# Kernel optimization log

Measured on AMD Instinct MI355X. Metric: run time of the kernel, lower is better.

Reference implementation:

```python
import jax, jax.numpy as jnp
import numpy as np
import math

M, D = 512, 512          # memory_size, feature_dim
B, H, W = 16, 64, 64     # conv feature map
TEMP_UPDATE, TEMP_GATHER = 0.1, 0.1


def _l2norm(x, axis):
    # torch F.normalize: x / clamp(||x||, min=eps)
    return x / jnp.maximum(jnp.linalg.norm(x, axis=axis, keepdims=True), 1e-12)


def setup_inputs() -> dict:
    key = jax.random.key(0)
    k1, k2 = jax.random.split(key)
    return {
        "query": jax.random.normal(k1, (B, D, H, W), jnp.float32),
        "keys": jax.random.normal(k2, (M, D), jnp.float32),
    }


def reference(query, keys):
    b, d, h, w = query.shape
    m = keys.shape[0]
    # L2-normalize over channel dim, then [b,h,w,d] -> flatten to [N,d]
    qn = _l2norm(query, 1)
    q = jnp.transpose(qn, (0, 2, 3, 1)).reshape(-1, d)  # [N, d]

    scale = math.sqrt(d) * max(TEMP_GATHER, 1e-6)
    logits = (q @ keys.T) / scale                       # [N, M]
    score_q = jax.nn.softmax(logits, axis=0)            # softmax over queries
    score_m = jax.nn.softmax(logits, axis=1)            # softmax over memory slots

    # ---- gather_loss (train) ----
    _, idx2 = jax.lax.top_k(score_m, 2)                 # [N, 2]
    pos = jax.lax.stop_gradient(keys[idx2[:, 0]])       # top-1 slot
    neg = jax.lax.stop_gradient(keys[idx2[:, 1]])       # top-2 slot (hard negative)
    compactness_loss = jnp.mean((q - pos) ** 2)
    # torch TripletMarginLoss(margin=1.0): pairwise_distance adds eps=1e-6 to diff
    dpos = jnp.linalg.norm(q - pos + 1e-6, axis=1)
    dneg = jnp.linalg.norm(q - neg + 1e-6, axis=1)
    separateness_loss = jnp.mean(jax.nn.relu(dpos - dneg + 1.0))

    # ---- read ----
    concat_mem = jax.lax.stop_gradient(score_m) @ keys  # [N, d]
    updated_query = jnp.concatenate([q, concat_mem], axis=1).reshape(b, h, w, 2 * d)
    updated_query = jnp.transpose(updated_query, (0, 3, 1, 2))  # [b, 2d, h, w]

    # ---- update (torch.no_grad) ----
    g = idx2[:, 0]                                              # gathering indices [N]
    wgt = jnp.take_along_axis(score_q, g[:, None], axis=1)[:, 0]
    query_update = jax.ops.segment_sum(q * wgt[:, None], g, num_segments=m)  # scatter-add
    mmt = min(max(1.0 / max(TEMP_UPDATE, 1e-6), 0.0), 0.999)
    updated_memory = _l2norm(keys * mmt + query_update * (1.0 - mmt), 1)
    updated_memory = jax.lax.stop_gradient(updated_memory)

    return (updated_query, updated_memory, score_q, score_m,
            separateness_loss, compactness_loss)
```

## Files before the change

### kernel.cpp

```cpp
#include <hip/hip_runtime.h>
#include <stdint.h>

#define UM_OFF   67108864u
#define SQ_OFF   67371008u
#define SM_OFF   100925440u
#define SEP_OFF  134479872u
#define COMP_OFF 134479873u

#define WS_QBF   0u
#define WS_EBF   67108864u
#define WS_KBF   134217728u
#define WS_KTBF  134742016u
#define WS_G     135266304u
#define WS_W     135528448u
#define WS_RSUM  135790592u
#define WS_CSUM  136052736u
#define WS_KN2   136054784u
#define WS_KSM   136056832u
#define WS_QSUM  136058880u

typedef __attribute__((ext_vector_type(8))) short short8v;
typedef __attribute__((ext_vector_type(4))) float float4v;

__device__ __forceinline__ unsigned short f2bf(float f) {
  union { float f; uint32_t u; } v; v.f = f;
  return (unsigned short)((v.u + 0x7fffu + ((v.u >> 16) & 1u)) >> 16);
}
__device__ __forceinline__ float bf2f(unsigned short s) {
  union { uint32_t u; float f; } v; v.u = ((uint32_t)s) << 16;
  return v.f;
}

#define GLDS16(gp, lp) __builtin_amdgcn_global_load_lds( \
    (__attribute__((address_space(1))) const void*)(gp), \
    (__attribute__((address_space(3))) void*)(lp), 16, 0, 0)

__global__ __launch_bounds__(512) void k01_prep_norm(
    const float* __restrict__ query, const float* __restrict__ keys,
    unsigned short* __restrict__ kbf, unsigned short* __restrict__ ktbf,
    float* __restrict__ csum, float* __restrict__ rsum,
    float* __restrict__ kn2, float* __restrict__ ksm,
    unsigned short* __restrict__ qbf, float* __restrict__ qsum,
    float* __restrict__ out) {
  int tid = threadIdx.x;
  if (blockIdx.x >= 1024) {
    __shared__ float pn[8], ps[8];
    int b = blockIdx.x - 1024;
    int t = tid;
    int i = b * 512 + t;
    float v = keys[i];
    kbf[i] = f2bf(v);
    ktbf[i] = f2bf(keys[(size_t)t * 512 + b]);
    float s1 = v, s2 = v * v;
    #pragma unroll
    for (int off = 1; off < 64; off <<= 1) {
      s1 += __shfl_xor(s1, off);
      s2 += __shfl_xor(s2, off);
    }
    if ((t & 63) == 0) { pn[t >> 6] = s2; ps[t >> 6] = s1; }
    __syncthreads();
    if (t == 0) {
      float n2 = 0.f, sm = 0.f;
      #pragma unroll
      for (int g = 0; g < 8; ++g) { n2 += pn[g]; sm += ps[g]; }
      kn2[b] = n2; ksm[b] = sm;
    }
    if (i < 65536) rsum[i] = 0.0f;
    if (i < 512) csum[i] = 0.0f;
    if (i < 2) out[SEP_OFF + i] = 0.0f;
    return;
  }
  __shared__ unsigned short vals[512 * 65];
  __shared__ float pp[8][64];
  __shared__ float rs[64];
  int bh = blockIdx.x;
  int b = bh >> 6, h = bh & 63;
  int w = tid & 63, dg = tid >> 6;
  const float* src = query + ((size_t)(b * 512) * 64 + h) * 64 + w;
  float ss = 0.f;
  #pragma unroll 4
  for (int i = 0; i < 64; ++i) {
    int d = dg * 64 + i;
    float v = src[(size_t)d * 4096];
    ss += v * v;
    vals[d * 65 + w] = f2bf(v);
  }
  pp[dg][w] = ss;
  __syncthreads();
  if (tid < 64) {
    float s = 0.f;
    #pragma unroll
    for (int g = 0; g < 8; ++g) s += pp[g][tid];
    rs[tid] = 1.0f / fmaxf(sqrtf(s), 1e-12f);
  }
  __syncthreads();
  float rw_ = rs[w];
  float* dst = out + ((size_t)(b * 1024) * 64 + h) * 64 + w;
  #pragma unroll 4
  for (int i = 0; i < 64; ++i) {
    int d = dg * 64 + i;
    __builtin_nontemporal_store(bf2f(vals[d * 65 + w]) * rw_, &dst[(size_t)d * 4096]);
  }
  int w2 = tid >> 3, dc = tid & 7;
  float rw = rs[w2];
  unsigned short* qrow = qbf + ((size_t)bh * 64 + w2) * 512;
  float qs = 0.f;
  #pragma unroll
  for (int g = 0; g < 8; ++g) {
    int d0 = g * 64 + dc * 8;
    short8v pk;
    #pragma unroll
    for (int jj = 0; jj < 8; ++jj) {
      float qn = bf2f(vals[(d0 + jj) * 65 + w2]) * rw;
      qs += qn;
      pk[jj] = (short)f2bf(qn);
    }
    *(short8v*)(qrow + d0) = pk;
  }
  qs += __shfl_xor(qs, 1); qs += __shfl_xor(qs, 2); qs += __shfl_xor(qs, 4);
  if (dc == 0) qsum[bh * 64 + w2] = qs;
}

__global__ __launch_bounds__(256) void k3_gemm1(
    const unsigned short* __restrict__ qbf, const unsigned short* __restrict__ kbf,
    unsigned short* __restrict__ ebf, float* __restrict__ csum, float* __restrict__ rsum) {
  __shared__ unsigned short As[128 * 32];
  __shared__ unsigned short Bs[128 * 32];
  int bid = blockIdx.x;
  int bm = (bid & 7) * 64 + (bid >> 5);
  int bn = (bid >> 3) & 3;
  int tid = threadIdx.x;
  int lane = tid & 63, wid = tid >> 6;
  int wr = wid >> 1, wc = wid & 1;
  float4v acc[4][4];
  #pragma unroll
  for (int m = 0; m < 4; ++m)
    #pragma unroll
    for (int n = 0; n < 4; ++n) acc[m][n] = (float4v){0.f, 0.f, 0.f, 0.f};
  const unsigned short* Abase = qbf + (size_t)bm * 128 * 512;
  const unsigned short* Bbase = kbf + (size_t)bn * 128 * 512;
  int u0 = wid * 128 + lane, u1 = u0 + 64;
  int ra0 = u0 >> 2, ca0 = (u0 & 3) * 8;
  int ra1 = u1 >> 2, ca1 = (u1 & 3) * 8;
  for (int kt = 0; kt < 16; ++kt) {
    const unsigned short* Ak = Abase + kt * 32;
    const unsigned short* Bk = Bbase + kt * 32;
    GLDS16(Ak + (size_t)ra0 * 512 + ca0, &As[(wid * 2 + 0) * 512]);
    GLDS16(Ak + (size_t)ra1 * 512 + ca1, &As[(wid * 2 + 1) * 512]);
    GLDS16(Bk + (size_t)ra0 * 512 + ca0, &Bs[(wid * 2 + 0) * 512]);
    GLDS16(Bk + (size_t)ra1 * 512 + ca1, &Bs[(wid * 2 + 1) * 512]);
    __syncthreads();
    short8v a[4], b[4];
    const unsigned short* pa = As + (wr * 64 + (lane & 15)) * 32 + (lane >> 4) * 8;
    const unsigned short* pb = Bs + (wc * 64 + (lane & 15)) * 32 + (lane >> 4) * 8;
    #pragma unroll
    for (int m = 0; m < 4; ++m) a[m] = *(const short8v*)(pa + m * 512);
    #pragma unroll
    for (int n = 0; n < 4; ++n) b[n] = *(const short8v*)(pb + n * 512);
    #pragma unroll
    for (int m = 0; m < 4; ++m)
      #pragma unroll
      for (int n = 0; n < 4; ++n)
        acc[m][n] = __builtin_amdgcn_mfma_f32_16x16x32_bf16(a[m], b[n], acc[m][n], 0, 0, 0);
    __syncthreads();
  }
  const float inv_scale = 0.44194173824159216f;
  int r0 = bm * 128 + wr * 64 + (lane >> 4) * 4;
  int c0 = bn * 128 + wc * 64 + (lane & 15);
  float cs[4] = {0.f, 0.f, 0.f, 0.f};
  float rp[4][4];
  #pragma unroll
  for (int m = 0; m < 4; ++m)
    #pragma unroll
    for (int j = 0; j < 4; ++j) rp[m][j] = 0.f;
  #pragma unroll
  for (int m = 0; m < 4; ++m)
    #pragma unroll
    for (int n = 0; n < 4; ++n)
      #pragma unroll
      for (int j = 0; j < 4; ++j) {
        float v = __expf(acc[m][n][j] * inv_scale);
        ebf[(size_t)(r0 + m * 16 + j) * 512 + c0 + n * 16] = f2bf(v);
        cs[n] += v;
        rp[m][j] += v;
      }
  #pragma unroll
  for (int n = 0; n < 4; ++n) {
    float v = cs[n];
    v += __shfl_xor(v, 16);
    v += __shfl_xor(v, 32);
    if ((lane >> 4) == 0) atomicAdd(&csum[c0 + n * 16], v);
  }
  #pragma unroll
  for (int m = 0; m < 4; ++m)
    #pragma unroll
    for (int j = 0; j < 4; ++j) {
      float v = rp[m][j];
      v += __shfl_xor(v, 1); v += __shfl_xor(v, 2);
      v += __shfl_xor(v, 4); v += __shfl_xor(v, 8);
      rp[m][j] = v;
    }
  int g16 = lane & 15;
  float myrp = 0.f;
  #pragma unroll
  for (int m = 0; m < 4; ++m)
    #pragma unroll
    for (int j = 0; j < 4; ++j)
      if (g16 == m * 4 + j) myrp = rp[m][j];
  atomicAdd(&rsum[r0 + (g16 >> 2) * 16 + (g16 & 3)], myrp);
}

__global__ __launch_bounds__(256) void k5_fused(
    const unsigned short* __restrict__ ktbf, const unsigned short* __restrict__ ebf,
    const float* __restrict__ rsum, const float* __restrict__ csum,
    const float* __restrict__ qsum, const float* __restrict__ kn2,
    const float* __restrict__ ksm, int* __restrict__ gidx, float* __restrict__ gw,
    float* __restrict__ out) {
  __shared__ unsigned short As[128 * 32];
  __shared__ unsigned short Bs[128 * 32];
  int bid = blockIdx.x;
  int g = (bid & 7) * 64 + (bid >> 5);
  int b = g >> 5, nt = g & 31, dt = (bid >> 3) & 3;
  int tid = threadIdx.x;
  int lane = tid & 63, wid = tid >> 6;
  int wr = wid >> 1, wc = wid & 1;
  float4v acc[4][4];
  #pragma unroll
  for (int m = 0; m < 4; ++m)
    #pragma unroll
    for (int n = 0; n < 4; ++n) acc[m][n] = (float4v){0.f, 0.f, 0.f, 0.f};
  const unsigned short* Abase = ktbf + (size_t)dt * 128 * 512;
  size_t brow0 = (size_t)g * 128;
  int u0 = wid * 128 + lane, u1 = u0 + 64;
  int ra0 = u0 >> 2, ca0 = (u0 & 3) * 8;
  int ra1 = u1 >> 2, ca1 = (u1 & 3) * 8;
  for (int kt = 0; kt < 16; ++kt) {
    GLDS16(Abase + (size_t)ra0 * 512 + kt * 32 + ca0, &As[(wid * 2 + 0) * 512]);
    GLDS16(Abase + (size_t)ra1 * 512 + kt * 32 + ca1, &As[(wid * 2 + 1) * 512]);
    GLDS16(ebf + (brow0 + ra0) * 512 + kt * 32 + ca0, &Bs[(wid * 2 + 0) * 512]);
    GLDS16(ebf + (brow0 + ra1) * 512 + kt * 32 + ca1, &Bs[(wid * 2 + 1) * 512]);
    __syncthreads();
    short8v a[4], bb[4];
    const unsigned short* pa = As + (wr * 64 + (lane & 15)) * 32 + (lane >> 4) * 8;
    const unsigned short* pb = Bs + (wc * 64 + (lane & 15)) * 32 + (lane >> 4) * 8;
    #pragma unroll
    for (int m = 0; m < 4; ++m) a[m] = *(const short8v*)(pa + m * 512);
    #pragma unroll
    for (int n = 0; n < 4; ++n) bb[n] = *(const short8v*)(pb + n * 512);
    #pragma unroll
    for (int m = 0; m < 4; ++m)
      #pragma unroll
      for (int n = 0; n < 4; ++n)
        acc[m][n] = __builtin_amdgcn_mfma_f32_16x16x32_bf16(a[m], bb[n], acc[m][n], 0, 0, 0);
    __syncthreads();
  }
  {
    float* dst = out + (size_t)b * 4194304 + (size_t)512 * 4096;
    int d0 = dt * 128 + wr * 64 + (lane >> 4) * 4;
    int c0 = nt * 128 + wc * 64 + (lane & 15);
    float invc[4];
    #pragma unroll
    for (int n = 0; n < 4; ++n) invc[n] = 1.0f / rsum[b * 4096 + c0 + n * 16];
    #pragma unroll
    for (int m = 0; m < 4; ++m)
      #pragma unroll
      for (int n = 0; n < 4; ++n)
        #pragma unroll
        for (int j = 0; j < 4; ++j)
          __builtin_nontemporal_store(acc[m][n][j] * invc[n],
              &dst[(size_t)(d0 + m * 16 + j) * 4096 + (c0 + n * 16)]);
  }
  float4v cA = *(const float4v*)(csum + lane * 8);
  float4v cB = *(const float4v*)(csum + lane * 8 + 4);
  float4v rcA, rcB;
  #pragma unroll
  for (int j = 0; j < 4; ++j) { rcA[j] = 1.0f / cA[j]; rcB[j] = 1.0f / cB[j]; }
  float closs = 0.f, sloss = 0.f;
  const float S2 = 4.525483399593904f;
  int r_base = g * 128 + dt * 32 + wid * 8;
  for (int it = 0; it < 8; ++it) {
    int r = r_base + it;
    short8v eb = *(const short8v*)(ebf + (size_t)r * 512 + lane * 8);
    float e[8];
    #pragma unroll
    for (int j = 0; j < 8; ++j) e[j] = bf2f((unsigned short)eb[j]);
    float invr = 1.0f / rsum[r];
    float v1 = -1.f, v2 = -2.f; int i1 = 0, i2 = 0;
    #pragma unroll
    for (int j = 0; j < 8; ++j) {
      float val = e[j]; int idx = lane * 8 + j;
      if (val > v1) { v2 = v1; i2 = i1; v1 = val; i1 = idx; }
      else if (val > v2) { v2 = val; i2 = idx; }
    }
    #pragma unroll
    for (int off = 1; off < 64; off <<= 1) {
      float ov1 = __shfl_xor(v1, off); int oi1 = __shfl_xor(i1, off);
      float ov2 = __shfl_xor(v2, off); int oi2 = __shfl_xor(i2, off);
      bool take = (ov1 > v1) || (ov1 == v1 && oi1 < i1);
      float av = take ? v1 : v2;  int ai = take ? i1 : i2;
      float bv = take ? ov2 : ov1; int bi = take ? oi2 : oi1;
      bool t2 = (bv > av) || (bv == av && bi < ai);
      v2 = t2 ? bv : av; i2 = t2 ? bi : ai;
      v1 = take ? ov1 : v1; i1 = take ? oi1 : i1;
    }
    float* SQrow = out + SQ_OFF + (size_t)r * 512;
    float* SMrow = out + SM_OFF + (size_t)r * 512;
    float4v sq0, sq1, sm0, sm1;
    #pragma unroll
    for (int j = 0; j < 4; ++j) {
      sq0[j] = e[j] * rcA[j];     sq1[j] = e[4 + j] * rcB[j];
      sm0[j] = e[j] * invr;       sm1[j] = e[4 + j] * invr;
    }
    __builtin_nontemporal_store(sq0, (float4v*)(SQrow + lane * 8));
    __builtin_nontemporal_store(sq1, (float4v*)(SQrow + lane * 8 + 4));
    __builtin_nontemporal_store(sm0, (float4v*)(SMrow + lane * 8));
    __builtin_nontemporal_store(sm1, (float4v*)(SMrow + lane * 8 + 4));
    float qs = qsum[r];
    float cp_row = 1.0f + kn2[i1] - S2 * __logf(v1);
    float dp2 = cp_row + 2e-6f * (qs - ksm[i1]) + 5.12e-10f;
    float cn_row = 1.0f + kn2[i2] - S2 * __logf(v2);
    float dn2 = cn_row + 2e-6f * (qs - ksm[i2]) + 5.12e-10f;
    closs += cp_row;
    sloss += fmaxf(sqrtf(dp2) - sqrtf(dn2) + 1.0f, 0.f);
    if (lane == 0) { gidx[r] = i1; gw[r] = v1 / csum[i1]; }
  }
  if (lane == 0) {
    atomicAdd(out + SEP_OFF, sloss * (1.0f / 65536.0f));
    atomicAdd(out + COMP_OFF, closs * (1.0f / (65536.0f * 512.0f)));
  }
}

__global__ __launch_bounds__(512) void k4b_gather(
    const int* __restrict__ gidx, const float* __restrict__ gw,
    const unsigned short* __restrict__ qbf, const float* __restrict__ keys,
    float* __restrict__ out) {
  __shared__ float red[8][512];
  __shared__ float wss[8];
  int m = blockIdx.x;
  int tid = threadIdx.x, lane = tid & 63, wid = tid >> 6;
  float acc[8] = {0.f, 0.f, 0.f, 0.f, 0.f, 0.f, 0.f, 0.f};
  for (int c = 0; c < 128; ++c) {
    int r0 = wid * 8192 + c * 64;
    int gv = gidx[r0 + lane];
    unsigned long long mask = __ballot(gv == m);
    while (mask) {
      int bb = __ffsll((long long)mask) - 1;
      mask &= mask - 1;
      int r = r0 + bb;
      float wv = gw[r];
      short8v qv = *(const short8v*)(qbf + (size_t)r * 512 + lane * 8);
      #pragma unroll
      for (int j = 0; j < 8; ++j) acc[j] += wv * bf2f((unsigned short)qv[j]);
    }
  }
  #pragma unroll
  for (int j = 0; j < 8; ++j) red[wid][lane * 8 + j] = acc[j];
  __syncthreads();
  int d0 = tid;
  float s = 0.f;
  #pragma unroll
  for (int g = 0; g < 8; ++g) s += red[g][d0];
  float v = keys[(size_t)m * 512 + d0] * 0.999f + s * 0.001f;
  float ss = v * v;
  #pragma unroll
  for (int off = 1; off < 64; off <<= 1) ss += __shfl_xor(ss, off);
  if (lane == 0) wss[wid] = ss;
  __syncthreads();
  float tot = 0.f;
  #pragma unroll
  for (int g = 0; g < 8; ++g) tot += wss[g];
  float rsn = 1.0f / fmaxf(sqrtf(tot), 1e-12f);
  out[UM_OFF + (size_t)m * 512 + d0] = v * rsn;
}

extern "C" void kernel_launch(void* const* d_in, const int* in_sizes, int n_in,
                              void* d_out, int out_size, void* d_ws, size_t ws_size,
                              hipStream_t stream) {
  const float* query = (const float*)d_in[0];
  const float* keys  = (const float*)d_in[1];
  float* out = (float*)d_out;
  char* ws = (char*)d_ws;
  unsigned short* qbf  = (unsigned short*)(ws + WS_QBF);
  unsigned short* ebf  = (unsigned short*)(ws + WS_EBF);
  unsigned short* kbf  = (unsigned short*)(ws + WS_KBF);
  unsigned short* ktbf = (unsigned short*)(ws + WS_KTBF);
  int*   gidx = (int*)(ws + WS_G);
  float* gw   = (float*)(ws + WS_W);
  float* rsum = (float*)(ws + WS_RSUM);
  float* csum = (float*)(ws + WS_CSUM);
  float* kn2  = (float*)(ws + WS_KN2);
  float* ksm  = (float*)(ws + WS_KSM);
  float* qsum = (float*)(ws + WS_QSUM);

  k01_prep_norm<<<dim3(1536), dim3(512), 0, stream>>>(
      query, keys, kbf, ktbf, csum, rsum, kn2, ksm, qbf, qsum, out);
  k3_gemm1<<<dim3(2048), dim3(256), 0, stream>>>(qbf, kbf, ebf, csum, rsum);
  k5_fused<<<dim3(2048), dim3(256), 0, stream>>>(
      ktbf, ebf, rsum, csum, qsum, kn2, ksm, gidx, gw, out);
  k4b_gather<<<dim3(512), dim3(512), 0, stream>>>(gidx, gw, qbf, keys, out);
}
```

Measured before the change: 421.1 us.

## Bucket query rows per memory slot instead of scanning all indices in gather

The fused softmax kernel now appends each row index to a per-slot list, using an atomic counter per memory slot, instead of writing a dense top-1 index array. The gather kernel then walks only its slot's list rather than having each of the 512 blocks scan all 65536 indices with ballots. This removes the redundant full scans. In exchange it adds atomics in the fused kernel and makes the summation order nondeterministic. Lists are capped at 1024 entries per slot, so a heavily skewed assignment would silently drop rows.

```diff
diff --git a/kernel.cpp b/kernel.cpp
--- a/kernel.cpp
+++ b/kernel.cpp
@@ -11,13 +11,14 @@
 #define WS_EBF   67108864u
 #define WS_KBF   134217728u
 #define WS_KTBF  134742016u
-#define WS_G     135266304u
-#define WS_W     135528448u
-#define WS_RSUM  135790592u
-#define WS_CSUM  136052736u
-#define WS_KN2   136054784u
-#define WS_KSM   136056832u
-#define WS_QSUM  136058880u
+#define WS_W     135266304u
+#define WS_RSUM  135528448u
+#define WS_CSUM  135790592u
+#define WS_KN2   135792640u
+#define WS_KSM   135794688u
+#define WS_CNT   135796736u
+#define WS_QSUM  135798784u
+#define WS_LIST  136060928u
 
 typedef __attribute__((ext_vector_type(8))) short short8v;
 typedef __attribute__((ext_vector_type(4))) float float4v;
@@ -39,7 +40,7 @@
     const float* __restrict__ query, const float* __restrict__ keys,
     unsigned short* __restrict__ kbf, unsigned short* __restrict__ ktbf,
     float* __restrict__ csum, float* __restrict__ rsum,
-    float* __restrict__ kn2, float* __restrict__ ksm,
+    float* __restrict__ kn2, float* __restrict__ ksm, int* __restrict__ cnt,
     unsigned short* __restrict__ qbf, float* __restrict__ qsum,
     float* __restrict__ out) {
   int tid = threadIdx.x;
@@ -66,7 +67,7 @@
       kn2[b] = n2; ksm[b] = sm;
     }
     if (i < 65536) rsum[i] = 0.0f;
-    if (i < 512) csum[i] = 0.0f;
+    if (i < 512) { csum[i] = 0.0f; cnt[i] = 0; }
     if (i < 2) out[SEP_OFF + i] = 0.0f;
     return;
   }
@@ -214,8 +215,8 @@
     const unsigned short* __restrict__ ktbf, const unsigned short* __restrict__ ebf,
     const float* __restrict__ rsum, const float* __restrict__ csum,
     const float* __restrict__ qsum, const float* __restrict__ kn2,
-    const float* __restrict__ ksm, int* __restrict__ gidx, float* __restrict__ gw,
-    float* __restrict__ out) {
+    const float* __restrict__ ksm, int* __restrict__ cnt, int* __restrict__ list,
+    float* __restrict__ gw, float* __restrict__ out) {
   __shared__ unsigned short As[128 * 32];
   __shared__ unsigned short Bs[128 * 32];
   int bid = blockIdx.x;
@@ -322,7 +323,11 @@
     float dn2 = cn_row + 2e-6f * (qs - ksm[i2]) + 5.12e-10f;
     closs += cp_row;
     sloss += fmaxf(sqrtf(dp2) - sqrtf(dn2) + 1.0f, 0.f);
-    if (lane == 0) { gidx[r] = i1; gw[r] = v1 / csum[i1]; }
+    if (lane == 0) {
+      gw[r] = v1 / csum[i1];
+      int pos = atomicAdd(&cnt[i1], 1);
+      if (pos < 1024) list[(i1 << 10) + pos] = r;
+    }
   }
   if (lane == 0) {
     atomicAdd(out + SEP_OFF, sloss * (1.0f / 65536.0f));
@@ -331,27 +336,21 @@
 }
 
 __global__ __launch_bounds__(512) void k4b_gather(
-    const int* __restrict__ gidx, const float* __restrict__ gw,
-    const unsigned short* __restrict__ qbf, const float* __restrict__ keys,
-    float* __restrict__ out) {
+    const int* __restrict__ cnt, const int* __restrict__ list,
+    const float* __restrict__ gw, const unsigned short* __restrict__ qbf,
+    const float* __restrict__ keys, float* __restrict__ out) {
   __shared__ float red[8][512];
   __shared__ float wss[8];
   int m = blockIdx.x;
   int tid = threadIdx.x, lane = tid & 63, wid = tid >> 6;
+  int n = cnt[m]; if (n > 1024) n = 1024;
   float acc[8] = {0.f, 0.f, 0.f, 0.f, 0.f, 0.f, 0.f, 0.f};
-  for (int c = 0; c < 128; ++c) {
-    int r0 = wid * 8192 + c * 64;
-    int gv = gidx[r0 + lane];
-    unsigned long long mask = __ballot(gv == m);
-    while (mask) {
-      int bb = __ffsll((long long)mask) - 1;
-      mask &= mask - 1;
-      int r = r0 + bb;
-      float wv = gw[r];
-      short8v qv = *(const short8v*)(qbf + (size_t)r * 512 + lane * 8);
-      #pragma unroll
-      for (int j = 0; j < 8; ++j) acc[j] += wv * bf2f((unsigned short)qv[j]);
-    }
+  for (int idx = wid; idx < n; idx += 8) {
+    int r = list[(m << 10) + idx];
+    float wv = gw[r];
+    short8v qv = *(const short8v*)(qbf + (size_t)r * 512 + lane * 8);
+    #pragma unroll
+    for (int j = 0; j < 8; ++j) acc[j] += wv * bf2f((unsigned short)qv[j]);
   }
   #pragma unroll
   for (int j = 0; j < 8; ++j) red[wid][lane * 8 + j] = acc[j];
@@ -384,18 +383,19 @@
   unsigned short* ebf  = (unsigned short*)(ws + WS_EBF);
   unsigned short* kbf  = (unsigned short*)(ws + WS_KBF);
   unsigned short* ktbf = (unsigned short*)(ws + WS_KTBF);
-  int*   gidx = (int*)(ws + WS_G);
   float* gw   = (float*)(ws + WS_W);
   float* rsum = (float*)(ws + WS_RSUM);
   float* csum = (float*)(ws + WS_CSUM);
   float* kn2  = (float*)(ws + WS_KN2);
   float* ksm  = (float*)(ws + WS_KSM);
+  int*   cnt  = (int*)(ws + WS_CNT);
   float* qsum = (float*)(ws + WS_QSUM);
+  int*   list = (int*)(ws + WS_LIST);
 
   k01_prep_norm<<<dim3(1536), dim3(512), 0, stream>>>(
-      query, keys, kbf, ktbf, csum, rsum, kn2, ksm, qbf, qsum, out);
+      query, keys, kbf, ktbf, csum, rsum, kn2, ksm, cnt, qbf, qsum, out);
   k3_gemm1<<<dim3(2048), dim3(256), 0, stream>>>(qbf, kbf, ebf, csum, rsum);
   k5_fused<<<dim3(2048), dim3(256), 0, stream>>>(
-      ktbf, ebf, rsum, csum, qsum, kn2, ksm, gidx, gw, out);
-  k4b_gather<<<dim3(512), dim3(512), 0, stream>>>(gidx, gw, qbf, keys, out);
-}
+      ktbf, ebf, rsum, csum, qsum, kn2, ksm, cnt, list, gw, out);
+  k4b_gather<<<dim3(512), dim3(512), 0, stream>>>(cnt, list, gw, qbf, keys, out);
+}
```

After: 404.4 us, median of 2. -4.0%, faster.
